# Kernel optimization log

Hardware: AMD Instinct MI355X
Metric: run time of the kernel (lower is better)

Reference implementation:

```python
import jax, jax.numpy as jnp
import numpy as np

N = 4096   # num_nodes
W = 12     # window_size
H = 256    # hidden_dim
P = 10     # prediction_horizon
E = 131072 # num edges (avg degree 32)


def setup_inputs() -> dict:
    key = jax.random.key(0)
    ks = jax.random.split(key, 12)
    return {
        "x": jax.random.normal(ks[0], (N, W), jnp.float32),
        "edge_index": jax.random.randint(ks[1], (2, E), 0, N, jnp.int32),
        "edge_weight": jax.random.uniform(ks[2], (E,), jnp.float32),
        "gcn_w": jax.random.normal(ks[3], (H,), jnp.float32) * 0.2,
        "ta_w": jax.random.normal(ks[4], (W * H, H), jnp.float32) * 0.02,
        "ta_b": jnp.zeros((H,), jnp.float32),
        "w_ih": jax.random.normal(ks[5], (3 * H, H), jnp.float32) * 0.05,
        "w_hh": jax.random.normal(ks[6], (3 * H, H), jnp.float32) * 0.05,
        "b_ih": jnp.zeros((3 * H,), jnp.float32),
        "b_hh": jnp.zeros((3 * H,), jnp.float32),
        "out_w": jax.random.normal(ks[7], (H,), jnp.float32) * 0.05,
        "out_b": jnp.zeros((1,), jnp.float32),
    }


def _laplacian(edge_index, edge_weight):
    # dense adjacency with self loops, symmetric normalization D^-1/2 (A+I)^T D^-1/2
    adj = jnp.zeros((N, N), edge_weight.dtype).at[edge_index[0], edge_index[1]].set(edge_weight)
    adj = adj + jnp.eye(N, dtype=edge_weight.dtype)
    d = jnp.power(adj.sum(1), -0.5)
    d = jnp.where(jnp.isinf(d), 0.0, d)
    # torch: adj.matmul(diag(d)).T.matmul(diag(d)) == ((adj * d[None,:]).T) * d[None,:]
    return (adj * d[None, :]).T * d[None, :]


def _gru_cell(x, h, w_ih, w_hh, b_ih, b_hh):
    gx = x @ w_ih.T + b_ih          # (N, 3H)
    gh = h @ w_hh.T + b_hh          # (N, 3H)
    xr, xz, xn = jnp.split(gx, 3, axis=-1)
    hr, hz, hn = jnp.split(gh, 3, axis=-1)
    r = jax.nn.sigmoid(xr + hr)
    z = jax.nn.sigmoid(xz + hz)
    n = jnp.tanh(xn + r * hn)
    return (1.0 - z) * n + z * h


def reference(x, edge_index, edge_weight, gcn_w, ta_w, ta_b,
              w_ih, w_hh, b_ih, b_hh, out_w, out_b):
    L = _laplacian(edge_index, edge_weight)  # fixed across all horizon steps

    def single_step(window, h):
        ax = L @ window                                   # (N, W)
        # outer product with weight vector + tanh, flattened per node
        g = jnp.tanh(ax[:, :, None] * gcn_w[None, None, :]).reshape(N, W * H)
        t = jax.nn.relu(g @ ta_w + ta_b)                  # (N, H)
        h2 = _gru_cell(t, h, w_ih, w_hh, b_ih, b_hh)      # (N, H)
        pred = h2 @ out_w + out_b[0]                      # (N,)
        return pred, h2

    def scan_step(carry, _):
        window, h = carry
        pred, h2 = single_step(window, h)
        new_window = jnp.concatenate(
            [window[:, 1:], jax.lax.stop_gradient(pred)[:, None]], axis=1)
        return (new_window, h2), pred

    h0 = jnp.zeros((N, H), x.dtype)
    _, preds = jax.lax.scan(scan_step, (x, h0), None, length=P)  # (P, N)
    return preds.T  # (N, P)
```

## Files before the change

### kernel.cpp

```cpp
#include <hip/hip_runtime.h>
#include <math.h>

#define NN 4096
#define WW 12
#define HH 256
#define PP 10
#define EE 131072
#define HS 262144
#define HMASK (HS-1)
#define TS 192
#define TA 8.0f
#define RS 22

typedef __attribute__((ext_vector_type(8))) _Float16 half8v;
typedef __attribute__((ext_vector_type(4))) _Float16 half4v;
typedef __attribute__((ext_vector_type(4))) float f32x4;

__device__ __forceinline__ float fast_tanh(float x){
  float e = __expf(2.0f*x);
  return 1.0f - 2.0f/(e+1.0f);
}
__device__ __forceinline__ float fast_sigmoid(float x){
  return 1.0f/(1.0f+__expf(-x));
}


__global__ void k_init(const float* __restrict__ x, int* keys, int* midx,
                       float* deg, int* cnt, float* ring, float* hA, int* count){
  int i = blockIdx.x*256 + threadIdx.x;
  if (i < HS){ keys[i] = -1; midx[i] = -1; }
  if (i < NN){ deg[i] = 0.0f; cnt[i] = 0; }
  if (i < NN*WW){ int n = i/WW, w = i - n*WW; ring[n*RS + w] = x[i]; }
  if (i < NN*HH) hA[i] = 0.0f;
  if (i == 0) *count = 0;
}

__global__ void k_insert(const int* __restrict__ ei, int* keys, int* midx){
  int e = blockIdx.x*256 + threadIdx.x;
  if (e >= EE) return;
  int key = ei[e]*NN + ei[EE+e];
  unsigned h = (((unsigned)key)*2654435761u >> 14) & HMASK;
  for(;;){
    int k = keys[h];
    if (k == key){ atomicMax(&midx[h], e); return; }
    if (k == -1){
      int old = atomicCAS(&keys[h], -1, key);
      if (old == -1 || old == key){ atomicMax(&midx[h], e); return; }
    }
    h = (h+1) & HMASK;
  }
}

__global__ void k_compact(const int* __restrict__ ei, const float* __restrict__ ew,
                          const int* __restrict__ keys, const int* __restrict__ midx,
                          int* wsrc, int* wdst, float* wwt,
                          float* deg, int* cnt, int* count){
  int e = blockIdx.x*256 + threadIdx.x;
  if (e >= EE) return;
  int src = ei[e], dst = ei[EE+e];
  int key = src*NN + dst;
  unsigned h = (((unsigned)key)*2654435761u >> 14) & HMASK;
  while (keys[h] != key) h = (h+1) & HMASK;
  if (midx[h] == e){
    int p = atomicAdd(count, 1);
    wsrc[p] = src; wdst[p] = dst; wwt[p] = ew[e];
    atomicAdd(&deg[src], ew[e]);
    atomicAdd(&cnt[dst], 1);
  }
}

__global__ __launch_bounds__(1024) void k_scan(const int* __restrict__ cnt,
                                               int* row_start, int* fill){
  __shared__ int sd[NN];
  int tid = threadIdx.x;
  for (int i = tid; i < NN; i += 1024) sd[i] = cnt[i];
  __syncthreads();
  for (int off = 1; off < NN; off <<= 1){
    int v[4];
    #pragma unroll
    for (int r = 0; r < 4; ++r){
      int i = tid + r*1024;
      v[r] = (i >= off) ? sd[i-off] : 0;
    }
    __syncthreads();
    #pragma unroll
    for (int r = 0; r < 4; ++r) sd[tid + r*1024] += v[r];
    __syncthreads();
  }
  for (int i = tid; i < NN; i += 1024){
    int incl = sd[i];
    row_start[i+1] = incl;
    fill[i] = incl - cnt[i];
  }
  if (tid == 0) row_start[0] = 0;
}

__global__ void k_scatter(const int* __restrict__ wsrc, const int* __restrict__ wdst,
                          const float* __restrict__ wwt, const float* __restrict__ deg,
                          int* fill, int* csr_src, float* csr_cf,
                          const int* __restrict__ count){
  int p = blockIdx.x*256 + threadIdx.x;
  if (p >= *count) return;
  int s = wsrc[p], d = wdst[p];
  float c = wwt[p] * (1.0f/sqrtf(deg[s]+1.0f)) * (1.0f/sqrtf(deg[d]+1.0f));
  int pos = atomicAdd(&fill[d], 1);
  csr_src[pos] = s;
  csr_cf[pos] = c;
}

__global__ __launch_bounds__(256) void k_tab(const float* __restrict__ gcn_w,
                                             const float* __restrict__ ta_w,
                                             _Float16* __restrict__ tab16){
  __shared__ float As[32][64];
  __shared__ float Bs[32][64];
  __shared__ float gws[256];
  int tid = threadIdx.x;
  int n0 = blockIdx.x*64;
  int m0 = blockIdx.y*64;
  int w  = blockIdx.z;
  gws[tid] = gcn_w[tid];
  __syncthreads();
  float acc[4][4] = {};
  int tm = tid >> 4, tn = tid & 15;
  const float astep = 2.0f*TA/TS;
  for (int k0 = 0; k0 < 256; k0 += 32){
    #pragma unroll
    for (int r = 0; r < 2; ++r){
      int f = tid + r*256;
      int kk = f >> 4, n4 = (f & 15)*4;
      *(float4*)&Bs[kk][n4] = *(const float4*)&ta_w[(w*256 + k0+kk)*HH + n0 + n4];
    }
    {
      int kk = tid >> 3;
      int mb = (tid & 7)*8;
      float gw = gws[k0 + kk];
      #pragma unroll
      for (int i2 = 0; i2 < 8; ++i2){
        float a = -TA + (float)(m0 + mb + i2)*astep;
        As[kk][mb+i2] = fast_tanh(a*gw);
      }
    }
    __syncthreads();
    #pragma unroll
    for (int kk = 0; kk < 32; ++kk){
      float4 a4 = *(float4*)&As[kk][tm*4];
      float4 b4 = *(float4*)&Bs[kk][tn*4];
      float a[4] = {a4.x,a4.y,a4.z,a4.w};
      float b[4] = {b4.x,b4.y,b4.z,b4.w};
      #pragma unroll
      for (int i = 0; i < 4; ++i)
        #pragma unroll
        for (int j = 0; j < 4; ++j)
          acc[i][j] = fmaf(a[i], b[j], acc[i][j]);
    }
    __syncthreads();
  }
  #pragma unroll
  for (int i = 0; i < 4; ++i){
    int row = m0 + tm*4 + i;
    if (row <= TS){
      #pragma unroll
      for (int j = 0; j < 4; ++j)
        tab16[((size_t)w*(TS+1) + row)*HH + n0 + tn*4 + j] = (_Float16)acc[i][j];
    }
  }
}

__global__ void k_wpack(const float* __restrict__ w_ih, const float* __restrict__ w_hh,
                        _Float16* __restrict__ wp){
  int idx = blockIdx.x*256 + threadIdx.x;
  int lane = idx & 63;
  int rest = idx >> 6;
  int ct = rest & 15; rest >>= 4;
  int g  = rest & 3;
  int ks = rest >> 2;
  int col = ct*16 + (lane & 15);
  int kb  = ks*32 + (lane >> 4)*8;
  _Float16 w8[8];
  #pragma unroll
  for (int j = 0; j < 8; ++j){
    int k = kb + j;
    float v;
    if      (g == 0) v = (k < 256) ? w_ih[col*HH + k]        : w_hh[col*HH + k - 256];
    else if (g == 1) v = (k < 256) ? w_ih[(256+col)*HH + k]  : w_hh[(256+col)*HH + k - 256];
    else if (g == 2) v = (k < 256) ? w_ih[(512+col)*HH + k]  : 0.0f;
    else             v = (k < 256) ? 0.0f                    : w_hh[(512+col)*HH + k - 256];
    w8[j] = (_Float16)v;
  }
  *(half8v*)&wp[(size_t)idx*8] = *(half8v*)w8;
}

__global__ __launch_bounds__(1024, 4) void k_step(
    const int* __restrict__ rowst, const int* __restrict__ csr_src,
    const float* __restrict__ csr_cf, const float* __restrict__ deg,
    float* __restrict__ ring, const _Float16* __restrict__ tab16,
    const float* __restrict__ ta_b,
    const float* __restrict__ hc, float* __restrict__ hnb,
    const _Float16* __restrict__ wp,
    const float* __restrict__ b_ih, const float* __restrict__ b_hh,
    const float* __restrict__ out_w, const float* __restrict__ out_b,
    float* __restrict__ out, int s){

  __shared__ __align__(16) _Float16 Xh[64][17][8];
  __shared__ __align__(16) _Float16 Xl[64][17][8];
  __shared__ __align__(16) float h_pad[16][260];
  __shared__ int   sidx[16][12];
  __shared__ float sfrac[16][12];

  const int tid = threadIdx.x;
  const int n0 = blockIdx.x*16;
  const int wv = tid >> 6, lane = tid & 63;

  const size_t fbase = (size_t)wv*64 + lane;
  half8v b0[2], b1[2], b2[2];

#define LOADB(KS, BUF)                                                        \
  {                                                                           \
    const int G2v = ((KS) < 8) ? 2 : 3;                                       \
    const size_t fb = fbase + (size_t)(KS)*4096;                              \
    b0[BUF] = *(const half8v*)&wp[fb*8];                                      \
    b1[BUF] = *(const half8v*)&wp[(fb + 1024)*8];                             \
    b2[BUF] = *(const half8v*)&wp[(fb + (size_t)G2v*1024)*8];                 \
  }

  LOADB(0, 0)

  {
    int row = tid >> 6;
    int c0 = (tid & 63)*4;
    float4 v = *(const float4*)(hc + (size_t)(n0+row)*HH + c0);
    *(float4*)&h_pad[row][c0] = v;
    float f[4] = {v.x,v.y,v.z,v.w};
    _Float16 h4[4], l4[4];
    #pragma unroll
    for (int j = 0; j < 4; ++j){
      h4[j] = (_Float16)f[j];
      l4[j] = (_Float16)(f[j] - (float)h4[j]);
    }
    int koct = 32 + (c0 >> 3), elem = c0 & 7;
    *(half4v*)&Xh[koct][row][elem] = *(half4v*)h4;
    *(half4v*)&Xl[koct][row][elem] = *(half4v*)l4;
  }
  if (lane < 48){
    int w = lane >> 2, g = lane & 3;
    int node = n0 + wv;
    float acc0 = 0.0f;
    if (g == 0){
      float dv2 = 1.0f/(deg[node] + 1.0f);
      acc0 = dv2*ring[(size_t)node*RS + s + w];
    }
    int e1 = rowst[node+1];
    for (int e = rowst[node] + g; e < e1; e += 4)
      acc0 += csr_cf[e]*ring[(size_t)csr_src[e]*RS + s + w];
    acc0 += __shfl_xor(acc0, 1, 64);
    acc0 += __shfl_xor(acc0, 2, 64);
    if (g == 0){
      float u = (acc0 + TA) * ((float)TS/(2.0f*TA));
      u = fminf(fmaxf(u, 0.0f), (float)TS - 0.0005f);
      int i = (int)u;
      sidx[wv][w] = i;
      sfrac[wv][w] = u - (float)i;
    }
  }
  __syncthreads();

  {
    int col = tid & 255;
    int r0 = (tid >> 8)*4;
    int koct = col >> 3, elem = col & 7;
    float tb = ta_b[col];
    #pragma unroll
    for (int rr = 0; rr < 4; ++rr){
      int r = r0 + rr;
      float acc0 = tb;
      #pragma unroll
      for (int w = 0; w < 12; ++w){
        const _Float16* pj = tab16 + ((size_t)w*(TS+1) + sidx[r][w])*HH + col;
        float v0 = (float)pj[0], v1 = (float)pj[HH];
        acc0 += v0 + sfrac[r][w]*(v1 - v0);
      }
      float tv = acc0 > 0.0f ? acc0 : 0.0f;
      _Float16 hh_ = (_Float16)tv;
      Xh[koct][r][elem] = hh_;
      Xl[koct][r][elem] = (_Float16)(tv - (float)hh_);
    }
  }
  __syncthreads();

  f32x4 acc[4];
  #pragma unroll
  for (int g = 0; g < 4; ++g) acc[g] = (f32x4){0.f,0.f,0.f,0.f};

  const int a_row = lane & 15, a_ko = lane >> 4;

  #pragma unroll
  for (int ks = 0; ks < 16; ++ks){
    const int cur = ks & 1, nxt = cur ^ 1;
    if (ks < 15) LOADB(ks+1, nxt)
    half8v ah = *(const half8v*)&Xh[ks*4 + a_ko][a_row][0];
    half8v al = *(const half8v*)&Xl[ks*4 + a_ko][a_row][0];
    const int G2 = (ks < 8) ? 2 : 3;
    acc[0]  = __builtin_amdgcn_mfma_f32_16x16x32_f16(ah, b0[cur], acc[0], 0,0,0);
    acc[0]  = __builtin_amdgcn_mfma_f32_16x16x32_f16(al, b0[cur], acc[0], 0,0,0);
    acc[1]  = __builtin_amdgcn_mfma_f32_16x16x32_f16(ah, b1[cur], acc[1], 0,0,0);
    acc[1]  = __builtin_amdgcn_mfma_f32_16x16x32_f16(al, b1[cur], acc[1], 0,0,0);
    acc[G2] = __builtin_amdgcn_mfma_f32_16x16x32_f16(ah, b2[cur], acc[G2], 0,0,0);
    acc[G2] = __builtin_amdgcn_mfma_f32_16x16x32_f16(al, b2[cur], acc[G2], 0,0,0);
  }
#undef LOADB
  __syncthreads();

  {
    const int ecl  = lane & 15;
    const int erow = (lane >> 4)*4;
    const int col  = wv*16 + ecl;
    float br  = b_ih[col]        + b_hh[col];
    float bz  = b_ih[col + HH]   + b_hh[col + HH];
    float bxn = b_ih[col + 2*HH];
    float bhn = b_hh[col + 2*HH];
    #pragma unroll
    for (int q = 0; q < 4; ++q){
      int row = erow + q;
      float r = fast_sigmoid(acc[0][q] + br);
      float z = fast_sigmoid(acc[1][q] + bz);
      float n = fast_tanh(acc[2][q] + bxn + r*(acc[3][q] + bhn));
      float hv = h_pad[row][col];
      float hp = (1.0f - z)*n + z*hv;
      hnb[(size_t)(n0+row)*HH + col] = hp;
      h_pad[row][col] = hp;
    }
  }
  __syncthreads();

  {
    int c0 = lane*4;
    float4 hv = *(const float4*)&h_pad[wv][c0];
    float4 w4 = *(const float4*)(out_w + c0);
    float sacc = hv.x*w4.x + hv.y*w4.y + hv.z*w4.z + hv.w*w4.w;
    sacc += __shfl_xor(sacc, 1, 64);
    sacc += __shfl_xor(sacc, 2, 64);
    sacc += __shfl_xor(sacc, 4, 64);
    sacc += __shfl_xor(sacc, 8, 64);
    sacc += __shfl_xor(sacc, 16, 64);
    sacc += __shfl_xor(sacc, 32, 64);
    if (lane == 0){
      float pv = sacc + out_b[0];
      out[(size_t)(n0+wv)*PP + s] = pv;
      ring[(size_t)(n0+wv)*RS + 12 + s] = pv;
    }
  }
}


extern "C" void kernel_launch(void* const* d_in, const int* in_sizes, int n_in,
                              void* d_out, int out_size, void* d_ws, size_t ws_size,
                              hipStream_t stream){
  const float* x     = (const float*)d_in[0];
  const int*   ei    = (const int*)  d_in[1];
  const float* ew    = (const float*)d_in[2];
  const float* gcn_w = (const float*)d_in[3];
  const float* ta_w  = (const float*)d_in[4];
  const float* ta_b  = (const float*)d_in[5];
  const float* w_ih  = (const float*)d_in[6];
  const float* w_hh  = (const float*)d_in[7];
  const float* b_ih  = (const float*)d_in[8];
  const float* b_hh  = (const float*)d_in[9];
  const float* out_w = (const float*)d_in[10];
  const float* out_b = (const float*)d_in[11];
  float* out = (float*)d_out;

  char* p = (char*)d_ws;
  _Float16* tab16   = (_Float16*)p; p += (size_t)12*(TS+1)*HH*2;
  int*      keys    = (int*)p;      p += (size_t)HS*4;
  int*      midx    = (int*)p;      p += (size_t)HS*4;
  int*      wsrc    = (int*)p;      p += (size_t)EE*4;
  int*      wdst    = (int*)p;      p += (size_t)EE*4;
  float*    wwt     = (float*)p;    p += (size_t)EE*4;
  int*      csr_src = (int*)p;      p += (size_t)EE*4;
  float*    csr_cf  = (float*)p;    p += (size_t)EE*4;
  float*    deg     = (float*)p;    p += (size_t)NN*4;
  int*      cnt     = (int*)p;      p += (size_t)NN*4;
  int*      fill    = (int*)p;      p += (size_t)NN*4;
  int*      rowst   = (int*)p;      p += (size_t)(NN+64)*4;
  int*      count   = (int*)p;      p += 256;
  float*    ring    = (float*)p;    p += (size_t)NN*RS*4;
  float*    hA      = (float*)p;    p += (size_t)NN*HH*4;
  float*    hB      = (float*)p;    p += (size_t)NN*HH*4;
  _Float16* wp      = (_Float16*)p; p += (size_t)16*4*16*64*8*2;

  k_init   <<<(NN*HH)/256, 256, 0, stream>>>(x, keys, midx, deg, cnt, ring, hA, count);
  k_insert <<<EE/256, 256, 0, stream>>>(ei, keys, midx);
  k_compact<<<EE/256, 256, 0, stream>>>(ei, ew, keys, midx, wsrc, wdst, wwt, deg, cnt, count);
  k_scan   <<<1, 1024, 0, stream>>>(cnt, rowst, fill);
  k_scatter<<<EE/256, 256, 0, stream>>>(wsrc, wdst, wwt, deg, fill, csr_src, csr_cf, count);
  k_wpack  <<<256, 256, 0, stream>>>(w_ih, w_hh, wp);
  k_tab    <<<dim3(HH/64, (TS+64)/64, WW), 256, 0, stream>>>(gcn_w, ta_w, tab16);

  for (int s = 0; s < PP; ++s){
    const float* hc  = (s & 1) ? hB : hA;
    float*       hnb = (s & 1) ? hA : hB;
    k_step<<<NN/16, 1024, 0, stream>>>(rowst, csr_src, csr_cf, deg, ring, tab16,
                                       ta_b, hc, hnb, wp,
                                       b_ih, b_hh, out_w, out_b, out, s);
  }
}
```

Measured before the change: 301.6 us.

## Interleave lookup table pairs, fuse weight packing into table kernel, vectorize init

Stores each table entry together with the next row's value so that the interpolation in the step kernel reads one 32-bit word instead of two separate half loads, and precomputes byte offsets for those reads. Moves the GRU weight packing into extra blocks of the table-building kernel, which removes one launch. Vectorizes the init kernel with 4-wide stores over fewer blocks, and raises the step kernel's launch_bounds occupancy hint from 4 to 8. The price is a table twice as large and possible register pressure from the stricter launch bound.

```diff
diff --git a/kernel.cpp b/kernel.cpp
--- a/kernel.cpp
+++ b/kernel.cpp
@@ -27,12 +27,24 @@
 
 __global__ void k_init(const float* __restrict__ x, int* keys, int* midx,
                        float* deg, int* cnt, float* ring, float* hA, int* count){
-  int i = blockIdx.x*256 + threadIdx.x;
-  if (i < HS){ keys[i] = -1; midx[i] = -1; }
-  if (i < NN){ deg[i] = 0.0f; cnt[i] = 0; }
-  if (i < NN*WW){ int n = i/WW, w = i - n*WW; ring[n*RS + w] = x[i]; }
-  if (i < NN*HH) hA[i] = 0.0f;
-  if (i == 0) *count = 0;
+  int t = blockIdx.x*256 + threadIdx.x;
+  int i4 = t*4;
+  if (i4 < HS){
+    int4 m1 = make_int4(-1,-1,-1,-1);
+    *(int4*)&keys[i4] = m1;
+    *(int4*)&midx[i4] = m1;
+  }
+  if (i4 < NN*HH) *(float4*)&hA[i4] = make_float4(0.f,0.f,0.f,0.f);
+  if (i4 < NN*WW){
+    #pragma unroll
+    for (int j = 0; j < 4; ++j){
+      int i = i4 + j;
+      int n = i/WW, w = i - n*WW;
+      ring[n*RS + w] = x[i];
+    }
+  }
+  if (t < NN){ deg[t] = 0.0f; cnt[t] = 0; }
+  if (t == 0) *count = 0;
 }
 
 __global__ void k_insert(const int* __restrict__ ei, int* keys, int* midx){
@@ -110,14 +122,44 @@
 
 __global__ __launch_bounds__(256) void k_tab(const float* __restrict__ gcn_w,
                                              const float* __restrict__ ta_w,
-                                             _Float16* __restrict__ tab16){
+                                             const float* __restrict__ w_ih,
+                                             const float* __restrict__ w_hh,
+                                             _Float16* __restrict__ tabp,
+                                             _Float16* __restrict__ wp){
+  int tid = threadIdx.x;
+  int w  = blockIdx.z;
+  if (w == 12){
+    int sb = blockIdx.y*4 + blockIdx.x;
+    #pragma unroll
+    for (int k = 0; k < 16; ++k){
+      int idx = sb*4096 + k*256 + tid;
+      int lane = idx & 63;
+      int rest = idx >> 6;
+      int ct = rest & 15; rest >>= 4;
+      int g  = rest & 3;
+      int ks = rest >> 2;
+      int col = ct*16 + (lane & 15);
+      int kb  = ks*32 + (lane >> 4)*8;
+      _Float16 w8[8];
+      #pragma unroll
+      for (int j = 0; j < 8; ++j){
+        int kk = kb + j;
+        float v;
+        if      (g == 0) v = (kk < 256) ? w_ih[col*HH + kk]        : w_hh[col*HH + kk - 256];
+        else if (g == 1) v = (kk < 256) ? w_ih[(256+col)*HH + kk]  : w_hh[(256+col)*HH + kk - 256];
+        else if (g == 2) v = (kk < 256) ? w_ih[(512+col)*HH + kk]  : 0.0f;
+        else             v = (kk < 256) ? 0.0f                     : w_hh[(512+col)*HH + kk - 256];
+        w8[j] = (_Float16)v;
+      }
+      *(half8v*)&wp[(size_t)idx*8] = *(half8v*)w8;
+    }
+    return;
+  }
   __shared__ float As[32][64];
   __shared__ float Bs[32][64];
   __shared__ float gws[256];
-  int tid = threadIdx.x;
   int n0 = blockIdx.x*64;
   int m0 = blockIdx.y*64;
-  int w  = blockIdx.z;
   gws[tid] = gcn_w[tid];
   __syncthreads();
   float acc[4][4] = {};
@@ -160,40 +202,21 @@
     int row = m0 + tm*4 + i;
     if (row <= TS){
       #pragma unroll
-      for (int j = 0; j < 4; ++j)
-        tab16[((size_t)w*(TS+1) + row)*HH + n0 + tn*4 + j] = (_Float16)acc[i][j];
-    }
-  }
-}
-
-__global__ void k_wpack(const float* __restrict__ w_ih, const float* __restrict__ w_hh,
-                        _Float16* __restrict__ wp){
-  int idx = blockIdx.x*256 + threadIdx.x;
-  int lane = idx & 63;
-  int rest = idx >> 6;
-  int ct = rest & 15; rest >>= 4;
-  int g  = rest & 3;
-  int ks = rest >> 2;
-  int col = ct*16 + (lane & 15);
-  int kb  = ks*32 + (lane >> 4)*8;
-  _Float16 w8[8];
-  #pragma unroll
-  for (int j = 0; j < 8; ++j){
-    int k = kb + j;
-    float v;
-    if      (g == 0) v = (k < 256) ? w_ih[col*HH + k]        : w_hh[col*HH + k - 256];
-    else if (g == 1) v = (k < 256) ? w_ih[(256+col)*HH + k]  : w_hh[(256+col)*HH + k - 256];
-    else if (g == 2) v = (k < 256) ? w_ih[(512+col)*HH + k]  : 0.0f;
-    else             v = (k < 256) ? 0.0f                    : w_hh[(512+col)*HH + k - 256];
-    w8[j] = (_Float16)v;
-  }
-  *(half8v*)&wp[(size_t)idx*8] = *(half8v*)w8;
-}
-
-__global__ __launch_bounds__(1024, 4) void k_step(
+      for (int j = 0; j < 4; ++j){
+        int h = n0 + tn*4 + j;
+        _Float16 v = (_Float16)acc[i][j];
+        size_t base = ((size_t)w*(TS+1) + row)*HH + h;
+        tabp[base*2 + 0] = v;
+        if (row > 0) tabp[(base - HH)*2 + 1] = v;
+      }
+    }
+  }
+}
+
+__global__ __launch_bounds__(1024, 8) void k_step(
     const int* __restrict__ rowst, const int* __restrict__ csr_src,
     const float* __restrict__ csr_cf, const float* __restrict__ deg,
-    float* __restrict__ ring, const _Float16* __restrict__ tab16,
+    float* __restrict__ ring, const _Float16* __restrict__ tabp,
     const float* __restrict__ ta_b,
     const float* __restrict__ hc, float* __restrict__ hnb,
     const _Float16* __restrict__ wp,
@@ -204,7 +227,7 @@
   __shared__ __align__(16) _Float16 Xh[64][17][8];
   __shared__ __align__(16) _Float16 Xl[64][17][8];
   __shared__ __align__(16) float h_pad[16][260];
-  __shared__ int   sidx[16][12];
+  __shared__ int   ioffs[16][12];
   __shared__ float sfrac[16][12];
 
   const int tid = threadIdx.x;
@@ -258,7 +281,7 @@
       float u = (acc0 + TA) * ((float)TS/(2.0f*TA));
       u = fminf(fmaxf(u, 0.0f), (float)TS - 0.0005f);
       int i = (int)u;
-      sidx[wv][w] = i;
+      ioffs[wv][w] = (int)((((unsigned)w*(TS+1) + (unsigned)i)*HH)*4u);
       sfrac[wv][w] = u - (float)i;
     }
   }
@@ -269,14 +292,17 @@
     int r0 = (tid >> 8)*4;
     int koct = col >> 3, elem = col & 7;
     float tb = ta_b[col];
+    const char* tb_base = (const char*)tabp;
     #pragma unroll
     for (int rr = 0; rr < 4; ++rr){
       int r = r0 + rr;
       float acc0 = tb;
       #pragma unroll
       for (int w = 0; w < 12; ++w){
-        const _Float16* pj = tab16 + ((size_t)w*(TS+1) + sidx[r][w])*HH + col;
-        float v0 = (float)pj[0], v1 = (float)pj[HH];
+        unsigned pp = *(const unsigned*)(tb_base + ioffs[r][w] + col*4);
+        _Float16 p2[2];
+        *(unsigned*)p2 = pp;
+        float v0 = (float)p2[0], v1 = (float)p2[1];
         acc0 += v0 + sfrac[r][w]*(v1 - v0);
       }
       float tv = acc0 > 0.0f ? acc0 : 0.0f;
@@ -370,7 +396,7 @@
   float* out = (float*)d_out;
 
   char* p = (char*)d_ws;
-  _Float16* tab16   = (_Float16*)p; p += (size_t)12*(TS+1)*HH*2;
+  _Float16* tabp    = (_Float16*)p; p += (size_t)12*(TS+1)*HH*4;
   int*      keys    = (int*)p;      p += (size_t)HS*4;
   int*      midx    = (int*)p;      p += (size_t)HS*4;
   int*      wsrc    = (int*)p;      p += (size_t)EE*4;
@@ -388,18 +414,17 @@
   float*    hB      = (float*)p;    p += (size_t)NN*HH*4;
   _Float16* wp      = (_Float16*)p; p += (size_t)16*4*16*64*8*2;
 
-  k_init   <<<(NN*HH)/256, 256, 0, stream>>>(x, keys, midx, deg, cnt, ring, hA, count);
+  k_init   <<<1024, 256, 0, stream>>>(x, keys, midx, deg, cnt, ring, hA, count);
   k_insert <<<EE/256, 256, 0, stream>>>(ei, keys, midx);
   k_compact<<<EE/256, 256, 0, stream>>>(ei, ew, keys, midx, wsrc, wdst, wwt, deg, cnt, count);
   k_scan   <<<1, 1024, 0, stream>>>(cnt, rowst, fill);
   k_scatter<<<EE/256, 256, 0, stream>>>(wsrc, wdst, wwt, deg, fill, csr_src, csr_cf, count);
-  k_wpack  <<<256, 256, 0, stream>>>(w_ih, w_hh, wp);
-  k_tab    <<<dim3(HH/64, (TS+64)/64, WW), 256, 0, stream>>>(gcn_w, ta_w, tab16);
+  k_tab    <<<dim3(HH/64, (TS+64)/64, WW+1), 256, 0, stream>>>(gcn_w, ta_w, w_ih, w_hh, tabp, wp);
 
   for (int s = 0; s < PP; ++s){
     const float* hc  = (s & 1) ? hB : hA;
     float*       hnb = (s & 1) ? hA : hB;
-    k_step<<<NN/16, 1024, 0, stream>>>(rowst, csr_src, csr_cf, deg, ring, tab16,
+    k_step<<<NN/16, 1024, 0, stream>>>(rowst, csr_src, csr_cf, deg, ring, tabp,
                                        ta_b, hc, hnb, wp,
                                        b_ih, b_hh, out_w, out_b, out, s);
   }
```

After: 301.7 us. No clear change (+0.0%).
